# Optimization experiments

Hardware: AMD Instinct MI355X
Metric: run time of the kernel (lower is better)

## Reference

```python
import jax, jax.numpy as jnp
import numpy as np

B, TQ, TK, D, H = 4, 2048, 2048, 512, 8
NEG = -1e9
LN_EPS = 1e-3  # Keras LayerNormalization default


def setup_inputs() -> dict:
    key = jax.random.key(0)
    ks = jax.random.split(key, 5)
    s = 0.02
    return {
        "queries": jax.random.normal(ks[0], (B, TQ, D), jnp.float32),
        "keys_in": jax.random.normal(ks[1], (B, TK, D), jnp.float32),
        "Wq": jax.random.normal(ks[2], (D, D), jnp.float32) * s,
        "bq": jnp.zeros((D,), jnp.float32),
        "Wk": jax.random.normal(ks[3], (D, D), jnp.float32) * s,
        "bk": jnp.zeros((D,), jnp.float32),
        "Wv": jax.random.normal(ks[4], (D, D), jnp.float32) * s,
        "bv": jnp.zeros((D,), jnp.float32),
        "gamma": jnp.ones((D,), jnp.float32),
        "beta": jnp.zeros((D,), jnp.float32),
    }


def reference(queries, keys_in, Wq, bq, Wk, bk, Wv, bv, gamma, beta):
    # Dense projections with relu activation (as in the original layer)
    Q = jax.nn.relu(queries @ Wq + bq)   # [B, Tq, D]
    K = jax.nn.relu(keys_in @ Wk + bk)   # [B, Tk, D]
    V = jax.nn.relu(keys_in @ Wv + bv)   # [B, Tk, D]

    b, tq, d = Q.shape
    tk = K.shape[1]
    dh = d // H
    # split_heads: tf.split(axis=-1)+concat(axis=0) == contiguous feature chunks per head
    Qh = Q.reshape(b, tq, H, dh)
    Kh = K.reshape(b, tk, H, dh)
    Vh = V.reshape(b, tk, H, dh)

    scores = jnp.einsum('bqhd,bkhd->bhqk', Qh, Kh) / jnp.sqrt(jnp.float32(dh))

    # key padding mask derived from per-head K content: sum(|K|) > 0 along dh
    kmask = jnp.sum(jnp.abs(Kh), axis=-1) > 0            # [B, Tk, H]
    kmask = jnp.transpose(kmask, (0, 2, 1))              # [B, H, Tk]
    scores = jnp.where(kmask[:, :, None, :], scores, NEG)

    attn = jax.nn.softmax(scores, axis=-1)               # [B, H, Tq, Tk]

    # query mask: zero out attention rows for all-zero query positions
    qmask = (jnp.sum(jnp.abs(Qh), axis=-1) > 0).astype(attn.dtype)  # [B, Tq, H]
    qmask = jnp.transpose(qmask, (0, 2, 1))              # [B, H, Tq]
    attn = attn * qmask[:, :, :, None]

    out = jnp.einsum('bhqk,bkhd->bqhd', attn, Vh).reshape(b, tq, d)

    # residual + LayerNorm (Keras default: last axis, eps=1e-3)
    res = out + queries
    mu = jnp.mean(res, axis=-1, keepdims=True)
    var = jnp.var(res, axis=-1, keepdims=True)
    return (res - mu) * jax.lax.rsqrt(var + LN_EPS) * gamma + beta
```

## Files before the change

kernel.cpp:

```cpp
#include <hip/hip_runtime.h>
#include <cstdint>

#define BB 4
#define TT 2048
#define DD 512
#define HH 8
#define DH 64
#define NT (TT / 64)

using bf16x8 = __attribute__((ext_vector_type(8))) __bf16;
using f32x4  = __attribute__((ext_vector_type(4))) float;
using f32x16 = __attribute__((ext_vector_type(16))) float;
using us8    = __attribute__((ext_vector_type(8))) unsigned short;
using us4    = __attribute__((ext_vector_type(4))) unsigned short;
using u32x2  = __attribute__((ext_vector_type(2))) unsigned int;

typedef const __attribute__((address_space(1))) unsigned int* as1cp;
typedef __attribute__((address_space(3))) unsigned int* as3p;

__device__ __forceinline__ void gload16(const void* g, void* l) {
  __builtin_amdgcn_global_load_lds((as1cp)(uintptr_t)g,
                                   (as3p)(unsigned int)(uintptr_t)l, 16, 0, 0);
}

__device__ __forceinline__ unsigned short f2bf(float x) {
  unsigned int u = __float_as_uint(x);
  u += 0x7fffu + ((u >> 16) & 1u);
  return (unsigned short)(u >> 16);
}
__device__ __forceinline__ float bf2f(unsigned short u) {
  return __uint_as_float(((unsigned int)u) << 16);
}
__device__ __forceinline__ f32x4 MFMA(bf16x8 a, bf16x8 b, f32x4 c) {
  return __builtin_amdgcn_mfma_f32_16x16x32_bf16(a, b, c, 0, 0, 0);
}
__device__ __forceinline__ f32x16 MFMA32(bf16x8 a, bf16x8 b, f32x16 c) {
  return __builtin_amdgcn_mfma_f32_32x32x16_bf16(a, b, c, 0, 0, 0);
}
__device__ __forceinline__ unsigned int cvtpk(float lo, float hi) {
  unsigned int r;
  asm("v_cvt_pk_bf16_f32 %0, %1, %2" : "=v"(r) : "v"(lo), "v"(hi));
  return r;
}

#define WAITVM(N) asm volatile("s_waitcnt vmcnt(" #N ")" ::: "memory")
#define RAWBAR() asm volatile("s_barrier" ::: "memory")

__global__ __launch_bounds__(256) void cvt_inputs(const float4* __restrict__ q,
                                                  const float4* __restrict__ k,
                                                  us4* __restrict__ qb,
                                                  us4* __restrict__ kb) {
  size_t i = (size_t)blockIdx.x * 256 + threadIdx.x;
  float4 a = q[i];
  us4 o; o[0] = f2bf(a.x); o[1] = f2bf(a.y); o[2] = f2bf(a.z); o[3] = f2bf(a.w);
  qb[i] = o;
  float4 b = k[i];
  us4 p; p[0] = f2bf(b.x); p[1] = f2bf(b.y); p[2] = f2bf(b.z); p[3] = f2bf(b.w);
  kb[i] = p;
}

__global__ __launch_bounds__(256) void cvt_w(const float* __restrict__ Wq,
                                             const float* __restrict__ Wk,
                                             const float* __restrict__ Wv,
                                             unsigned short* __restrict__ Wt) {
  __shared__ float tile[32][33];
  int z = blockIdx.z;
  const float* W = (z == 0) ? Wq : (z == 1) ? Wk : Wv;
  int k0 = blockIdx.x * 32, n0 = blockIdx.y * 32;
  int r = threadIdx.x >> 5, c = threadIdx.x & 31;
#pragma unroll
  for (int p = 0; p < 4; ++p)
    tile[r + p * 8][c] = W[(size_t)(k0 + r + p * 8) * DD + n0 + c];
  __syncthreads();
  unsigned short* o = Wt + (size_t)z * DD * DD;
#pragma unroll
  for (int p = 0; p < 4; ++p)
    o[(size_t)(n0 + r + p * 8) * DD + k0 + c] = f2bf(tile[c][r + p * 8]);
}

__global__ __launch_bounds__(256) void gemm_proj(const unsigned short* __restrict__ qb,
                                                 const unsigned short* __restrict__ kb,
                                                 const unsigned short* __restrict__ Wt,
                                                 const float* __restrict__ bq,
                                                 const float* __restrict__ bk,
                                                 const float* __restrict__ bv,
                                                 unsigned short* __restrict__ Qp,
                                                 unsigned short* __restrict__ Kp,
                                                 unsigned short* __restrict__ Vp) {
  int z = blockIdx.z;
  const unsigned short* A  = (z == 0) ? qb : kb;
  const unsigned short* Bt = Wt + (size_t)z * DD * DD;
  const float* bias = (z == 0) ? bq : (z == 1) ? bk : bv;
  unsigned short* out = (z == 0) ? Qp : (z == 1) ? Kp : Vp;
  const float osc = (z == 0) ? 0.125f : 1.0f;

  __shared__ __align__(16) unsigned short As[128 * 32];
  __shared__ __align__(16) unsigned short Bs[128 * 32];

  int mb = blockIdx.x * 128, nb = blockIdx.y * 128;
  int w = threadIdx.x >> 6, lane = threadIdx.x & 63;
  int l15 = lane & 15, lg = lane >> 4;
  int wr = (w >> 1) * 64, wc = (w & 1) * 64;

  f32x4 acc[4][4] = {};

  for (int kt = 0; kt < DD / 32; ++kt) {
    int kk = kt * 32;
    int t = threadIdx.x;
#pragma unroll
    for (int it = 0; it < 2; ++it) {
      int c = t + it * 256;
      gload16(A  + (size_t)(mb + (c >> 2)) * DD + kk + (c & 3) * 8, As + c * 8);
      gload16(Bt + (size_t)(nb + (c >> 2)) * DD + kk + (c & 3) * 8, Bs + c * 8);
    }
    __syncthreads();
    bf16x8 af[4], bf[4];
#pragma unroll
    for (int m = 0; m < 4; ++m)
      af[m] = *(const bf16x8*)&As[(wr + m * 16 + l15) * 32 + lg * 8];
#pragma unroll
    for (int n = 0; n < 4; ++n)
      bf[n] = *(const bf16x8*)&Bs[(wc + n * 16 + l15) * 32 + lg * 8];
#pragma unroll
    for (int m = 0; m < 4; ++m)
#pragma unroll
      for (int n = 0; n < 4; ++n)
        acc[m][n] = MFMA(af[m], bf[n], acc[m][n]);
    __syncthreads();
  }

#pragma unroll
  for (int m = 0; m < 4; ++m)
#pragma unroll
    for (int n = 0; n < 4; ++n)
#pragma unroll
      for (int i = 0; i < 4; ++i) {
        int row = mb + wr + m * 16 + lg * 4 + i;
        int col = nb + wc + n * 16 + l15;
        float v = acc[m][n][i] + bias[col];
        out[(size_t)row * DD + col] = f2bf(fmaxf(v, 0.f) * osc);
      }
}

__global__ __launch_bounds__(256) void transpose_v(const unsigned short* __restrict__ Vp,
                                                   unsigned short* __restrict__ Vt) {
  __shared__ unsigned short tile[64][72];
  int b = blockIdx.z, k0 = blockIdx.x * 64, d0 = blockIdx.y * 64;
  int t = threadIdx.x;
  int r = t >> 3, c8 = (t & 7) * 8;
#pragma unroll
  for (int p = 0; p < 2; ++p) {
    int row = r + p * 32;
    us8 v = *(const us8*)&Vp[(size_t)(b * TT + k0 + row) * DD + d0 + c8];
#pragma unroll
    for (int j = 0; j < 8; ++j) tile[row][c8 + j] = v[j];
  }
  __syncthreads();
#pragma unroll
  for (int p = 0; p < 2; ++p) {
    int dr = r + p * 32;
    us8 o;
#pragma unroll
    for (int j = 0; j < 8; ++j) o[j] = tile[c8 + j][dr];
    *(us8*)&Vt[((size_t)b * DD + d0 + dr) * TT + k0 + c8] = o;
  }
}

__global__ __launch_bounds__(256) void mask_kernel(const unsigned short* __restrict__ Qp,
                                                   const unsigned short* __restrict__ Kp,
                                                   float* __restrict__ qmask,
                                                   uint2* __restrict__ kbits) {
  int id = blockIdx.x * 4 + (threadIdx.x >> 6);
  int lane = threadIdx.x & 63;
  int side = id >> 10;
  int rem = id & 1023;
  int bh = rem >> 5, tile = rem & 31;
  int b = bh >> 3, h = bh & 7;
  const unsigned short* src =
      (side ? Kp : Qp) + ((size_t)(b * TT + tile * 64 + lane)) * DD + h * DH;
  float s = 0.f;
#pragma unroll
  for (int j = 0; j < 64; j += 8) {
    us8 v = *(const us8*)(src + j);
#pragma unroll
    for (int e = 0; e < 8; ++e) s += bf2f(v[e]);
  }
  if (side == 0) {
    qmask[(size_t)bh * TT + tile * 64 + lane] = (s > 0.f) ? 1.f : 0.f;
  } else {
    unsigned long long mb = __ballot(s > 0.f);
    if (lane == 0)
      kbits[bh * NT + tile] = make_uint2((unsigned int)mb, (unsigned int)(mb >> 32));
  }
}

#define PV_SLOT(SS, base, ks)                                               \
  {                                                                         \
    unsigned int w0_ = cvtpk(SS[(base) + 0], SS[(base) + 1]);               \
    unsigned int w1_ = cvtpk(SS[(base) + 2], SS[(base) + 3]);               \
    unsigned int w2_ = cvtpk(SS[(base) + 4], SS[(base) + 5]);               \
    unsigned int w3_ = cvtpk(SS[(base) + 6], SS[(base) + 7]);               \
    u32x2 r20_ = __builtin_amdgcn_permlane32_swap(w2_, w0_, false, false);  \
    u32x2 r31_ = __builtin_amdgcn_permlane32_swap(w3_, w1_, false, false);  \
    union { unsigned int u[4]; bf16x8 v; } pa_;                             \
    pa_.u[0] = r20_[1]; pa_.u[1] = r31_[1];                                 \
    pa_.u[2] = r20_[0]; pa_.u[3] = r31_[0];                                 \
    oat0 = MFMA32(vf0[(ks)], pa_.v, oat0);                                  \
    oat1 = MFMA32(vf1[(ks)], pa_.v, oat1);                                  \
  }

#define STAGE(tt, pb)                                                        \
  {                                                                          \
    int c0_ = threadIdx.x;                                                   \
    _Pragma("unroll")                                                        \
    for (int it_ = 0; it_ < 2; ++it_) {                                      \
      int c_ = c0_ + it_ * 256;                                              \
      int r_ = c_ >> 3, j_ = c_ & 7;                                         \
      int js_ = j_ ^ (r_ & 7);                                               \
      gload16(kg + (size_t)((tt) * 64 + r_) * DD + js_ * 8,                  \
              &KsBuf[pb][(size_t)c_ * 8]);                                   \
      gload16(vg + (size_t)r_ * TT + (tt) * 64 + js_ * 8,                    \
              &VsBuf[pb][(size_t)c_ * 8]);                                   \
    }                                                                        \
  }

__global__ __launch_bounds__(256) void attn_kernel(
    const unsigned short* __restrict__ Qp,
    const unsigned short* __restrict__ Kp,
    const unsigned short* __restrict__ Vt,
    const uint2* __restrict__ kbits,
    const float* __restrict__ qmask,
    float* __restrict__ O) {
  __shared__ __align__(16) unsigned short KsBuf[2][64 * 64];
  __shared__ __align__(16) unsigned short VsBuf[2][64 * 64];

  const int w = threadIdx.x >> 6;
  const int lane = threadIdx.x & 63;
  const int l31 = lane & 31, h2 = lane >> 5;

  int flat = blockIdx.x;
  int wg = (flat & 7) * 64 + (flat >> 3);
  int qt = wg & 15, bh = wg >> 4;
  int h = bh & 7, b = bh >> 3;
  int q0 = qt * 128 + w * 32;

  const unsigned short* qbase =
      Qp + ((size_t)(b * TT + q0 + l31)) * DD + h * DH + h2 * 8;
  bf16x8 qf[4];
#pragma unroll
  for (int kd = 0; kd < 4; ++kd) qf[kd] = *(const bf16x8*)(qbase + kd * 16);

  const unsigned short* kg = Kp + ((size_t)b * TT) * DD + h * DH;
  const unsigned short* vg = Vt + ((size_t)(b * DD + h * DH)) * TT;
  const uint2* kb_ptr = kbits + (size_t)bh * NT;

  f32x16 oat0 = {}, oat1 = {};
  float m_i = -1e30f, l_i = 0.f;

  STAGE(0, 0);

  for (int t = 0; t < NT; ++t) {
    int pb = t & 1;
    if (t + 1 < NT) {
      STAGE(t + 1, pb ^ 1);
      WAITVM(4);
    } else {
      WAITVM(0);
    }
    RAWBAR();

    const unsigned short* ksb = &KsBuf[pb][0];
    const unsigned short* vsb = &VsBuf[pb][0];

    bf16x8 kf0[4], kf1[4];
#pragma unroll
    for (int kd = 0; kd < 4; ++kd) {
      int j = kd * 2 + h2;
      int r0 = l31, r1 = 32 + l31;
      kf0[kd] = *(const bf16x8*)&ksb[((size_t)r0 * 8 + (j ^ (r0 & 7))) * 8];
      kf1[kd] = *(const bf16x8*)&ksb[((size_t)r1 * 8 + (j ^ (r1 & 7))) * 8];
    }

    f32x16 s0 = {}, s1 = {};
    __builtin_amdgcn_s_setprio(1);
#pragma unroll
    for (int kd = 0; kd < 4; ++kd) s0 = MFMA32(kf0[kd], qf[kd], s0);
#pragma unroll
    for (int kd = 0; kd < 4; ++kd) s1 = MFMA32(kf1[kd], qf[kd], s1);
    __builtin_amdgcn_s_setprio(0);

    bf16x8 vf0[4], vf1[4];
#pragma unroll
    for (int ks = 0; ks < 4; ++ks) {
      int j = ks * 2 + h2;
      int r0 = l31, r1 = 32 + l31;
      vf0[ks] = *(const bf16x8*)&vsb[((size_t)r0 * 8 + (j ^ (r0 & 7))) * 8];
      vf1[ks] = *(const bf16x8*)&vsb[((size_t)r1 * 8 + (j ^ (r1 & 7))) * 8];
    }

    uint2 kw = kb_ptr[t];
    if ((kw.x & kw.y) != 0xffffffffu) {
      unsigned int w0s = kw.x >> (h2 * 4), w1s = kw.y >> (h2 * 4);
#pragma unroll
      for (int r = 0; r < 16; ++r) {
        int bi = (r & 3) + 8 * (r >> 2);
        if (!((w0s >> bi) & 1)) s0[r] = -1e30f;
        if (!((w1s >> bi) & 1)) s1[r] = -1e30f;
      }
    }

    float x0 = fmaxf(fmaxf(fmaxf(s0[0], s0[1]), fmaxf(s0[2], s0[3])),
                     fmaxf(fmaxf(s0[4], s0[5]), fmaxf(s0[6], s0[7])));
    float x1 = fmaxf(fmaxf(fmaxf(s0[8], s0[9]), fmaxf(s0[10], s0[11])),
                     fmaxf(fmaxf(s0[12], s0[13]), fmaxf(s0[14], s0[15])));
    float x2 = fmaxf(fmaxf(fmaxf(s1[0], s1[1]), fmaxf(s1[2], s1[3])),
                     fmaxf(fmaxf(s1[4], s1[5]), fmaxf(s1[6], s1[7])));
    float x3 = fmaxf(fmaxf(fmaxf(s1[8], s1[9]), fmaxf(s1[10], s1[11])),
                     fmaxf(fmaxf(s1[12], s1[13]), fmaxf(s1[14], s1[15])));
    float pm = fmaxf(fmaxf(x0, x1), fmaxf(x2, x3));
    u32x2 sw = __builtin_amdgcn_permlane32_swap(__float_as_uint(pm),
                                                __float_as_uint(pm), false, false);
    pm = fmaxf(__uint_as_float(sw[0]), __uint_as_float(sw[1]));

    if (__any(pm > m_i + 8.f)) {
      float mn = fmaxf(m_i, pm);
      float al = __expf(m_i - mn);
      m_i = mn;
      l_i *= al;
#pragma unroll
      for (int r = 0; r < 16; ++r) { oat0[r] *= al; oat1[r] *= al; }
    }

    float a0 = 0.f, a1 = 0.f, a2 = 0.f, a3 = 0.f;
#pragma unroll
    for (int r = 0; r < 8; ++r)  { float p = __expf(s0[r] - m_i); s0[r] = p; a0 += p; }
#pragma unroll
    for (int r = 8; r < 16; ++r) { float p = __expf(s0[r] - m_i); s0[r] = p; a1 += p; }
#pragma unroll
    for (int r = 0; r < 8; ++r)  { float p = __expf(s1[r] - m_i); s1[r] = p; a2 += p; }
#pragma unroll
    for (int r = 8; r < 16; ++r) { float p = __expf(s1[r] - m_i); s1[r] = p; a3 += p; }
    float rs = (a0 + a1) + (a2 + a3);
    u32x2 sr = __builtin_amdgcn_permlane32_swap(__float_as_uint(rs),
                                                __float_as_uint(rs), false, false);
    rs = __uint_as_float(sr[0]) + __uint_as_float(sr[1]);
    l_i += rs;

    __builtin_amdgcn_s_setprio(1);
    PV_SLOT(s0, 0, 0)
    PV_SLOT(s0, 8, 1)
    PV_SLOT(s1, 0, 2)
    PV_SLOT(s1, 8, 3)
    __builtin_amdgcn_s_setprio(0);

    if (t + 1 < NT) RAWBAR();
  }

  float qm = qmask[(size_t)bh * TT + q0 + l31];
  float sc = qm / l_i;
  float* ob = O + ((size_t)(b * TT + q0 + l31)) * DD + h * DH + h2 * 4;
#pragma unroll
  for (int qq = 0; qq < 4; ++qq) {
    float4 v0 = make_float4(oat0[4 * qq + 0] * sc, oat0[4 * qq + 1] * sc,
                            oat0[4 * qq + 2] * sc, oat0[4 * qq + 3] * sc);
    *(float4*)(ob + 8 * qq) = v0;
    float4 v1 = make_float4(oat1[4 * qq + 0] * sc, oat1[4 * qq + 1] * sc,
                            oat1[4 * qq + 2] * sc, oat1[4 * qq + 3] * sc);
    *(float4*)(ob + 32 + 8 * qq) = v1;
  }
}

__global__ __launch_bounds__(256) void ln_kernel(const float* __restrict__ O,
                                                 const float* __restrict__ qin,
                                                 const float* __restrict__ gamma,
                                                 const float* __restrict__ beta,
                                                 float* __restrict__ out) {
  int row = blockIdx.x * 4 + (threadIdx.x >> 6);
  int lane = threadIdx.x & 63;
  size_t base = (size_t)row * DD + lane * 8;
  const float4* o4 = (const float4*)(O + base);
  const float4* q4 = (const float4*)(qin + base);
  float4 a = o4[0], b2 = o4[1], c = q4[0], d2 = q4[1];
  float v[8];
  v[0] = a.x + c.x; v[1] = a.y + c.y; v[2] = a.z + c.z; v[3] = a.w + c.w;
  v[4] = b2.x + d2.x; v[5] = b2.y + d2.y; v[6] = b2.z + d2.z; v[7] = b2.w + d2.w;
  float s = 0.f, s2 = 0.f;
#pragma unroll
  for (int j = 0; j < 8; ++j) { s += v[j]; s2 += v[j] * v[j]; }
#pragma unroll
  for (int xm = 1; xm < 64; xm <<= 1) {
    s += __shfl_xor(s, xm);
    s2 += __shfl_xor(s2, xm);
  }
  float mu = s * (1.0f / DD);
  float var = s2 * (1.0f / DD) - mu * mu;
  float rs = rsqrtf(var + 1e-3f);
  const float* g = gamma + lane * 8;
  const float* bb = beta + lane * 8;
  float* ob = out + base;
#pragma unroll
  for (int j = 0; j < 8; ++j) ob[j] = (v[j] - mu) * rs * g[j] + bb[j];
}

extern "C" void kernel_launch(void* const* d_in, const int* in_sizes, int n_in,
                              void* d_out, int out_size, void* d_ws, size_t ws_size,
                              hipStream_t stream) {
  (void)in_sizes; (void)n_in; (void)out_size; (void)ws_size;
  const float* queries = (const float*)d_in[0];
  const float* keys_in = (const float*)d_in[1];
  const float* Wq = (const float*)d_in[2];
  const float* bq = (const float*)d_in[3];
  const float* Wk = (const float*)d_in[4];
  const float* bk = (const float*)d_in[5];
  const float* Wv = (const float*)d_in[6];
  const float* bv = (const float*)d_in[7];
  const float* gamma = (const float*)d_in[8];
  const float* beta  = (const float*)d_in[9];
  float* out = (float*)d_out;

  char* ws = (char*)d_ws;
  unsigned short* qb = (unsigned short*)(ws);
  unsigned short* kb = (unsigned short*)(ws + (8ull << 20));
  float*          O  = (float*)(ws);
  unsigned short* Qp = (unsigned short*)(ws + (16ull << 20));
  unsigned short* Kp = (unsigned short*)(ws + (24ull << 20));
  unsigned short* Vp = (unsigned short*)(ws + (32ull << 20));
  unsigned short* Vt = (unsigned short*)(ws + (40ull << 20));
  unsigned short* Wt = (unsigned short*)(ws + (48ull << 20));
  float* qmaskp = (float*)(ws + (50ull << 20));
  uint2* kbitsp = (uint2*)(ws + (50ull << 20) + (512ull << 10));

  cvt_inputs<<<4096, 256, 0, stream>>>((const float4*)queries, (const float4*)keys_in,
                                       (us4*)qb, (us4*)kb);
  cvt_w<<<dim3(16, 16, 3), 256, 0, stream>>>(Wq, Wk, Wv, Wt);
  gemm_proj<<<dim3(64, 4, 3), 256, 0, stream>>>(qb, kb, Wt, bq, bk, bv, Qp, Kp, Vp);
  transpose_v<<<dim3(32, 8, 4), 256, 0, stream>>>(Vp, Vt);
  mask_kernel<<<512, 256, 0, stream>>>(Qp, Kp, qmaskp, kbitsp);
  attn_kernel<<<512, 256, 0, stream>>>(Qp, Kp, Vt, kbitsp, qmaskp, O);
  ln_kernel<<<2048, 256, 0, stream>>>(O, queries, gamma, beta, out);
}
```

Before: 193.8 us.

## Switch attention to 16x16 MFMA tiles, exp2 softmax, and merge small prep kernels

Replaces the 32x32x16 MFMA attention inner loop with 16x16x32 tiles. Each wave now handles 16 queries instead of 32, so the launch grows to 1024 blocks of 64 queries each. Softmax moves to exp2 by folding log2(e) into the Q scale, with a clamp and a larger rescale threshold. Separately, the input/weight conversion kernels are merged into one launch, and the V transpose and mask kernels into another, to cut launch overhead. The smaller tiles give more parallelism but lower per-wave reuse of K/V tiles and more LDS traffic.

```diff
diff --git a/kernel.cpp b/kernel.cpp
--- a/kernel.cpp
+++ b/kernel.cpp
@@ -7,10 +7,10 @@
 #define HH 8
 #define DH 64
 #define NT (TT / 64)
+#define LOG2E 1.4426950408889634f
 
 using bf16x8 = __attribute__((ext_vector_type(8))) __bf16;
 using f32x4  = __attribute__((ext_vector_type(4))) float;
-using f32x16 = __attribute__((ext_vector_type(16))) float;
 using us8    = __attribute__((ext_vector_type(8))) unsigned short;
 using us4    = __attribute__((ext_vector_type(4))) unsigned short;
 using u32x2  = __attribute__((ext_vector_type(2))) unsigned int;
@@ -34,48 +34,43 @@
 __device__ __forceinline__ f32x4 MFMA(bf16x8 a, bf16x8 b, f32x4 c) {
   return __builtin_amdgcn_mfma_f32_16x16x32_bf16(a, b, c, 0, 0, 0);
 }
-__device__ __forceinline__ f32x16 MFMA32(bf16x8 a, bf16x8 b, f32x16 c) {
-  return __builtin_amdgcn_mfma_f32_32x32x16_bf16(a, b, c, 0, 0, 0);
-}
-__device__ __forceinline__ unsigned int cvtpk(float lo, float hi) {
-  unsigned int r;
-  asm("v_cvt_pk_bf16_f32 %0, %1, %2" : "=v"(r) : "v"(lo), "v"(hi));
-  return r;
-}
 
 #define WAITVM(N) asm volatile("s_waitcnt vmcnt(" #N ")" ::: "memory")
 #define RAWBAR() asm volatile("s_barrier" ::: "memory")
 
-__global__ __launch_bounds__(256) void cvt_inputs(const float4* __restrict__ q,
-                                                  const float4* __restrict__ k,
-                                                  us4* __restrict__ qb,
-                                                  us4* __restrict__ kb) {
-  size_t i = (size_t)blockIdx.x * 256 + threadIdx.x;
-  float4 a = q[i];
-  us4 o; o[0] = f2bf(a.x); o[1] = f2bf(a.y); o[2] = f2bf(a.z); o[3] = f2bf(a.w);
-  qb[i] = o;
-  float4 b = k[i];
-  us4 p; p[0] = f2bf(b.x); p[1] = f2bf(b.y); p[2] = f2bf(b.z); p[3] = f2bf(b.w);
-  kb[i] = p;
-}
-
-__global__ __launch_bounds__(256) void cvt_w(const float* __restrict__ Wq,
-                                             const float* __restrict__ Wk,
-                                             const float* __restrict__ Wv,
-                                             unsigned short* __restrict__ Wt) {
+__global__ __launch_bounds__(256) void prep_kernel(const float4* __restrict__ q,
+                                                   const float4* __restrict__ k,
+                                                   us4* __restrict__ qb,
+                                                   us4* __restrict__ kb,
+                                                   const float* __restrict__ Wq,
+                                                   const float* __restrict__ Wk,
+                                                   const float* __restrict__ Wv,
+                                                   unsigned short* __restrict__ Wt) {
   __shared__ float tile[32][33];
-  int z = blockIdx.z;
-  const float* W = (z == 0) ? Wq : (z == 1) ? Wk : Wv;
-  int k0 = blockIdx.x * 32, n0 = blockIdx.y * 32;
-  int r = threadIdx.x >> 5, c = threadIdx.x & 31;
-#pragma unroll
-  for (int p = 0; p < 4; ++p)
-    tile[r + p * 8][c] = W[(size_t)(k0 + r + p * 8) * DD + n0 + c];
-  __syncthreads();
-  unsigned short* o = Wt + (size_t)z * DD * DD;
-#pragma unroll
-  for (int p = 0; p < 4; ++p)
-    o[(size_t)(n0 + r + p * 8) * DD + k0 + c] = f2bf(tile[c][r + p * 8]);
+  int id = blockIdx.x;
+  if (id < 4096) {
+    size_t i = (size_t)id * 256 + threadIdx.x;
+    float4 a = q[i];
+    us4 o; o[0] = f2bf(a.x); o[1] = f2bf(a.y); o[2] = f2bf(a.z); o[3] = f2bf(a.w);
+    qb[i] = o;
+    float4 b = k[i];
+    us4 p; p[0] = f2bf(b.x); p[1] = f2bf(b.y); p[2] = f2bf(b.z); p[3] = f2bf(b.w);
+    kb[i] = p;
+  } else {
+    int id2 = id - 4096;
+    int z = id2 >> 8, rem = id2 & 255;
+    const float* W = (z == 0) ? Wq : (z == 1) ? Wk : Wv;
+    int k0 = (rem & 15) * 32, n0 = (rem >> 4) * 32;
+    int r = threadIdx.x >> 5, c = threadIdx.x & 31;
+#pragma unroll
+    for (int p = 0; p < 4; ++p)
+      tile[r + p * 8][c] = W[(size_t)(k0 + r + p * 8) * DD + n0 + c];
+    __syncthreads();
+    unsigned short* o = Wt + (size_t)z * DD * DD;
+#pragma unroll
+    for (int p = 0; p < 4; ++p)
+      o[(size_t)(n0 + r + p * 8) * DD + k0 + c] = f2bf(tile[c][r + p * 8]);
+  }
 }
 
 __global__ __launch_bounds__(256) void gemm_proj(const unsigned short* __restrict__ qb,
@@ -92,7 +87,7 @@
   const unsigned short* Bt = Wt + (size_t)z * DD * DD;
   const float* bias = (z == 0) ? bq : (z == 1) ? bk : bv;
   unsigned short* out = (z == 0) ? Qp : (z == 1) ? Kp : Vp;
-  const float osc = (z == 0) ? 0.125f : 1.0f;
+  const float osc = (z == 0) ? 0.125f * LOG2E : 1.0f;
 
   __shared__ __align__(16) unsigned short As[128 * 32];
   __shared__ __align__(16) unsigned short Bs[128 * 32];
@@ -142,74 +137,61 @@
       }
 }
 
-__global__ __launch_bounds__(256) void transpose_v(const unsigned short* __restrict__ Vp,
-                                                   unsigned short* __restrict__ Vt) {
+__global__ __launch_bounds__(256) void post_proj(const unsigned short* __restrict__ Qp,
+                                                 const unsigned short* __restrict__ Kp,
+                                                 const unsigned short* __restrict__ Vp,
+                                                 unsigned short* __restrict__ Vt,
+                                                 float* __restrict__ qmask,
+                                                 uint2* __restrict__ kbits) {
   __shared__ unsigned short tile[64][72];
-  int b = blockIdx.z, k0 = blockIdx.x * 64, d0 = blockIdx.y * 64;
-  int t = threadIdx.x;
-  int r = t >> 3, c8 = (t & 7) * 8;
-#pragma unroll
-  for (int p = 0; p < 2; ++p) {
-    int row = r + p * 32;
-    us8 v = *(const us8*)&Vp[(size_t)(b * TT + k0 + row) * DD + d0 + c8];
-#pragma unroll
-    for (int j = 0; j < 8; ++j) tile[row][c8 + j] = v[j];
-  }
-  __syncthreads();
-#pragma unroll
-  for (int p = 0; p < 2; ++p) {
-    int dr = r + p * 32;
-    us8 o;
-#pragma unroll
-    for (int j = 0; j < 8; ++j) o[j] = tile[c8 + j][dr];
-    *(us8*)&Vt[((size_t)b * DD + d0 + dr) * TT + k0 + c8] = o;
-  }
-}
-
-__global__ __launch_bounds__(256) void mask_kernel(const unsigned short* __restrict__ Qp,
-                                                   const unsigned short* __restrict__ Kp,
-                                                   float* __restrict__ qmask,
-                                                   uint2* __restrict__ kbits) {
-  int id = blockIdx.x * 4 + (threadIdx.x >> 6);
-  int lane = threadIdx.x & 63;
-  int side = id >> 10;
-  int rem = id & 1023;
-  int bh = rem >> 5, tile = rem & 31;
-  int b = bh >> 3, h = bh & 7;
-  const unsigned short* src =
-      (side ? Kp : Qp) + ((size_t)(b * TT + tile * 64 + lane)) * DD + h * DH;
-  float s = 0.f;
-#pragma unroll
-  for (int j = 0; j < 64; j += 8) {
-    us8 v = *(const us8*)(src + j);
-#pragma unroll
-    for (int e = 0; e < 8; ++e) s += bf2f(v[e]);
-  }
-  if (side == 0) {
-    qmask[(size_t)bh * TT + tile * 64 + lane] = (s > 0.f) ? 1.f : 0.f;
+  int id = blockIdx.x;
+  if (id < 1024) {
+    int b = id >> 8, k0 = (id & 31) * 64, d0 = ((id >> 5) & 7) * 64;
+    int t = threadIdx.x;
+    int r = t >> 3, c8 = (t & 7) * 8;
+#pragma unroll
+    for (int p = 0; p < 2; ++p) {
+      int row = r + p * 32;
+      us8 v = *(const us8*)&Vp[(size_t)(b * TT + k0 + row) * DD + d0 + c8];
+#pragma unroll
+      for (int j = 0; j < 8; ++j) tile[row][c8 + j] = v[j];
+    }
+    __syncthreads();
+#pragma unroll
+    for (int p = 0; p < 2; ++p) {
+      int dr = r + p * 32;
+      us8 o;
+#pragma unroll
+      for (int j = 0; j < 8; ++j) o[j] = tile[c8 + j][dr];
+      *(us8*)&Vt[((size_t)b * DD + d0 + dr) * TT + k0 + c8] = o;
+    }
   } else {
-    unsigned long long mb = __ballot(s > 0.f);
-    if (lane == 0)
-      kbits[bh * NT + tile] = make_uint2((unsigned int)mb, (unsigned int)(mb >> 32));
-  }
-}
-
-#define PV_SLOT(SS, base, ks)                                               \
-  {                                                                         \
-    unsigned int w0_ = cvtpk(SS[(base) + 0], SS[(base) + 1]);               \
-    unsigned int w1_ = cvtpk(SS[(base) + 2], SS[(base) + 3]);               \
-    unsigned int w2_ = cvtpk(SS[(base) + 4], SS[(base) + 5]);               \
-    unsigned int w3_ = cvtpk(SS[(base) + 6], SS[(base) + 7]);               \
-    u32x2 r20_ = __builtin_amdgcn_permlane32_swap(w2_, w0_, false, false);  \
-    u32x2 r31_ = __builtin_amdgcn_permlane32_swap(w3_, w1_, false, false);  \
-    union { unsigned int u[4]; bf16x8 v; } pa_;                             \
-    pa_.u[0] = r20_[1]; pa_.u[1] = r31_[1];                                 \
-    pa_.u[2] = r20_[0]; pa_.u[3] = r31_[0];                                 \
-    oat0 = MFMA32(vf0[(ks)], pa_.v, oat0);                                  \
-    oat1 = MFMA32(vf1[(ks)], pa_.v, oat1);                                  \
-  }
-
-#define STAGE(tt, pb)                                                        \
+    int wid = (id - 1024) * 4 + (threadIdx.x >> 6);
+    int lane = threadIdx.x & 63;
+    int side = wid >> 10;
+    int rem = wid & 1023;
+    int bh = rem >> 5, tl = rem & 31;
+    int b = bh >> 3, h = bh & 7;
+    const unsigned short* src =
+        (side ? Kp : Qp) + ((size_t)(b * TT + tl * 64 + lane)) * DD + h * DH;
+    float s = 0.f;
+#pragma unroll
+    for (int j = 0; j < 64; j += 8) {
+      us8 v = *(const us8*)(src + j);
+#pragma unroll
+      for (int e = 0; e < 8; ++e) s += bf2f(v[e]);
+    }
+    if (side == 0) {
+      qmask[(size_t)bh * TT + tl * 64 + lane] = (s > 0.f) ? 1.f : 0.f;
+    } else {
+      unsigned long long mb = __ballot(s > 0.f);
+      if (lane == 0)
+        kbits[bh * NT + tl] = make_uint2((unsigned int)mb, (unsigned int)(mb >> 32));
+    }
+  }
+}
+
+#define STAGE(tt, pbuf)                                                      \
   {                                                                          \
     int c0_ = threadIdx.x;                                                   \
     _Pragma("unroll")                                                        \
@@ -218,9 +200,9 @@
       int r_ = c_ >> 3, j_ = c_ & 7;                                         \
       int js_ = j_ ^ (r_ & 7);                                               \
       gload16(kg + (size_t)((tt) * 64 + r_) * DD + js_ * 8,                  \
-              &KsBuf[pb][(size_t)c_ * 8]);                                   \
+              &KsBuf[pbuf][(size_t)c_ * 8]);                                 \
       gload16(vg + (size_t)r_ * TT + (tt) * 64 + js_ * 8,                    \
-              &VsBuf[pb][(size_t)c_ * 8]);                                   \
+              &VsBuf[pbuf][(size_t)c_ * 8]);                                 \
     }                                                                        \
   }
 
@@ -236,25 +218,26 @@
 
   const int w = threadIdx.x >> 6;
   const int lane = threadIdx.x & 63;
-  const int l31 = lane & 31, h2 = lane >> 5;
+  const int l15 = lane & 15, lg = lane >> 4;
 
   int flat = blockIdx.x;
-  int wg = (flat & 7) * 64 + (flat >> 3);
-  int qt = wg & 15, bh = wg >> 4;
+  int wg = (flat & 7) * 128 + (flat >> 3);
+  int qt = wg & 31, bh = wg >> 5;
   int h = bh & 7, b = bh >> 3;
-  int q0 = qt * 128 + w * 32;
+  int q0 = qt * 64 + w * 16;
 
   const unsigned short* qbase =
-      Qp + ((size_t)(b * TT + q0 + l31)) * DD + h * DH + h2 * 8;
-  bf16x8 qf[4];
-#pragma unroll
-  for (int kd = 0; kd < 4; ++kd) qf[kd] = *(const bf16x8*)(qbase + kd * 16);
+      Qp + ((size_t)(b * TT + q0 + l15)) * DD + h * DH + lg * 8;
+  bf16x8 qf0 = *(const bf16x8*)(qbase);
+  bf16x8 qf1 = *(const bf16x8*)(qbase + 32);
 
   const unsigned short* kg = Kp + ((size_t)b * TT) * DD + h * DH;
   const unsigned short* vg = Vt + ((size_t)(b * DD + h * DH)) * TT;
   const uint2* kb_ptr = kbits + (size_t)bh * NT;
 
-  f32x16 oat0 = {}, oat1 = {};
+  const int krow_base = ((l15 & 12) << 1) | (l15 & 3);
+
+  f32x4 oat[4] = {};
   float m_i = -1e30f, l_i = 0.f;
 
   STAGE(0, 0);
@@ -272,101 +255,105 @@
     const unsigned short* ksb = &KsBuf[pb][0];
     const unsigned short* vsb = &VsBuf[pb][0];
 
-    bf16x8 kf0[4], kf1[4];
-#pragma unroll
-    for (int kd = 0; kd < 4; ++kd) {
-      int j = kd * 2 + h2;
-      int r0 = l31, r1 = 32 + l31;
-      kf0[kd] = *(const bf16x8*)&ksb[((size_t)r0 * 8 + (j ^ (r0 & 7))) * 8];
-      kf1[kd] = *(const bf16x8*)&ksb[((size_t)r1 * 8 + (j ^ (r1 & 7))) * 8];
-    }
-
-    f32x16 s0 = {}, s1 = {};
+    f32x4 s[4];
     __builtin_amdgcn_s_setprio(1);
 #pragma unroll
-    for (int kd = 0; kd < 4; ++kd) s0 = MFMA32(kf0[kd], qf[kd], s0);
-#pragma unroll
-    for (int kd = 0; kd < 4; ++kd) s1 = MFMA32(kf1[kd], qf[kd], s1);
+    for (int f = 0; f < 4; ++f) {
+      int row = krow_base + ((f & 1) << 2) + ((f >> 1) << 5);
+      int r7 = row & 7;
+      bf16x8 k0 = *(const bf16x8*)&ksb[row * 64 + ((lg ^ r7) << 3)];
+      bf16x8 k1 = *(const bf16x8*)&ksb[row * 64 + (((4 | lg) ^ r7) << 3)];
+      f32x4 z = {};
+      z = MFMA(k0, qf0, z);
+      s[f] = MFMA(k1, qf1, z);
+    }
     __builtin_amdgcn_s_setprio(0);
 
-    bf16x8 vf0[4], vf1[4];
-#pragma unroll
-    for (int ks = 0; ks < 4; ++ks) {
-      int j = ks * 2 + h2;
-      int r0 = l31, r1 = 32 + l31;
-      vf0[ks] = *(const bf16x8*)&vsb[((size_t)r0 * 8 + (j ^ (r0 & 7))) * 8];
-      vf1[ks] = *(const bf16x8*)&vsb[((size_t)r1 * 8 + (j ^ (r1 & 7))) * 8];
+    bf16x8 vf[4][2];
+#pragma unroll
+    for (int fd = 0; fd < 4; ++fd) {
+      int row = 16 * fd + l15;
+      int r7 = l15 & 7;
+      vf[fd][0] = *(const bf16x8*)&vsb[row * 64 + ((lg ^ r7) << 3)];
+      vf[fd][1] = *(const bf16x8*)&vsb[row * 64 + (((4 | lg) ^ r7) << 3)];
     }
 
     uint2 kw = kb_ptr[t];
     if ((kw.x & kw.y) != 0xffffffffu) {
-      unsigned int w0s = kw.x >> (h2 * 4), w1s = kw.y >> (h2 * 4);
-#pragma unroll
-      for (int r = 0; r < 16; ++r) {
-        int bi = (r & 3) + 8 * (r >> 2);
-        if (!((w0s >> bi) & 1)) s0[r] = -1e30f;
-        if (!((w1s >> bi) & 1)) s1[r] = -1e30f;
+#pragma unroll
+      for (int f = 0; f < 4; ++f) {
+        unsigned int word = (f >> 1) ? kw.y : kw.x;
+        unsigned int nib = (word >> (8 * lg + 4 * (f & 1))) & 0xFu;
+#pragma unroll
+        for (int i = 0; i < 4; ++i)
+          if (!((nib >> i) & 1)) s[f][i] = -1e30f;
       }
     }
 
-    float x0 = fmaxf(fmaxf(fmaxf(s0[0], s0[1]), fmaxf(s0[2], s0[3])),
-                     fmaxf(fmaxf(s0[4], s0[5]), fmaxf(s0[6], s0[7])));
-    float x1 = fmaxf(fmaxf(fmaxf(s0[8], s0[9]), fmaxf(s0[10], s0[11])),
-                     fmaxf(fmaxf(s0[12], s0[13]), fmaxf(s0[14], s0[15])));
-    float x2 = fmaxf(fmaxf(fmaxf(s1[0], s1[1]), fmaxf(s1[2], s1[3])),
-                     fmaxf(fmaxf(s1[4], s1[5]), fmaxf(s1[6], s1[7])));
-    float x3 = fmaxf(fmaxf(fmaxf(s1[8], s1[9]), fmaxf(s1[10], s1[11])),
-                     fmaxf(fmaxf(s1[12], s1[13]), fmaxf(s1[14], s1[15])));
-    float pm = fmaxf(fmaxf(x0, x1), fmaxf(x2, x3));
+    float m0 = fmaxf(fmaxf(s[0][0], s[0][1]), fmaxf(s[0][2], s[0][3]));
+    float m1 = fmaxf(fmaxf(s[1][0], s[1][1]), fmaxf(s[1][2], s[1][3]));
+    float m2 = fmaxf(fmaxf(s[2][0], s[2][1]), fmaxf(s[2][2], s[2][3]));
+    float m3 = fmaxf(fmaxf(s[3][0], s[3][1]), fmaxf(s[3][2], s[3][3]));
+    float pm = fmaxf(fmaxf(m0, m1), fmaxf(m2, m3));
+    pm = fmaxf(pm, __shfl_xor(pm, 16));
     u32x2 sw = __builtin_amdgcn_permlane32_swap(__float_as_uint(pm),
                                                 __float_as_uint(pm), false, false);
     pm = fmaxf(__uint_as_float(sw[0]), __uint_as_float(sw[1]));
 
-    if (__any(pm > m_i + 8.f)) {
+    if (__any(pm > m_i + 12.f)) {
       float mn = fmaxf(m_i, pm);
-      float al = __expf(m_i - mn);
+      float al = exp2f(m_i - mn);
       m_i = mn;
       l_i *= al;
 #pragma unroll
-      for (int r = 0; r < 16; ++r) { oat0[r] *= al; oat1[r] *= al; }
-    }
-
-    float a0 = 0.f, a1 = 0.f, a2 = 0.f, a3 = 0.f;
-#pragma unroll
-    for (int r = 0; r < 8; ++r)  { float p = __expf(s0[r] - m_i); s0[r] = p; a0 += p; }
-#pragma unroll
-    for (int r = 8; r < 16; ++r) { float p = __expf(s0[r] - m_i); s0[r] = p; a1 += p; }
-#pragma unroll
-    for (int r = 0; r < 8; ++r)  { float p = __expf(s1[r] - m_i); s1[r] = p; a2 += p; }
-#pragma unroll
-    for (int r = 8; r < 16; ++r) { float p = __expf(s1[r] - m_i); s1[r] = p; a3 += p; }
-    float rs = (a0 + a1) + (a2 + a3);
-    u32x2 sr = __builtin_amdgcn_permlane32_swap(__float_as_uint(rs),
-                                                __float_as_uint(rs), false, false);
-    rs = __uint_as_float(sr[0]) + __uint_as_float(sr[1]);
-    l_i += rs;
+      for (int f = 0; f < 4; ++f)
+#pragma unroll
+        for (int i = 0; i < 4; ++i) oat[f][i] *= al;
+    }
+
+    float a = 0.f;
+#pragma unroll
+    for (int f = 0; f < 4; ++f)
+#pragma unroll
+      for (int i = 0; i < 4; ++i) {
+        float p = exp2f(fminf(s[f][i] - m_i, 30.f));
+        s[f][i] = p;
+        a += p;
+      }
+    a += __shfl_xor(a, 16);
+    u32x2 sr = __builtin_amdgcn_permlane32_swap(__float_as_uint(a),
+                                                __float_as_uint(a), false, false);
+    a = __uint_as_float(sr[0]) + __uint_as_float(sr[1]);
+    l_i += a;
+
+    bf16x8 pb0v, pb1v;
+#pragma unroll
+    for (int f2 = 0; f2 < 2; ++f2)
+#pragma unroll
+      for (int i = 0; i < 4; ++i) {
+        pb0v[f2 * 4 + i] = (__bf16)s[f2][i];
+        pb1v[f2 * 4 + i] = (__bf16)s[2 + f2][i];
+      }
 
     __builtin_amdgcn_s_setprio(1);
-    PV_SLOT(s0, 0, 0)
-    PV_SLOT(s0, 8, 1)
-    PV_SLOT(s1, 0, 2)
-    PV_SLOT(s1, 8, 3)
+#pragma unroll
+    for (int fd = 0; fd < 4; ++fd) {
+      oat[fd] = MFMA(vf[fd][0], pb0v, oat[fd]);
+      oat[fd] = MFMA(vf[fd][1], pb1v, oat[fd]);
+    }
     __builtin_amdgcn_s_setprio(0);
 
     if (t + 1 < NT) RAWBAR();
   }
 
-  float qm = qmask[(size_t)bh * TT + q0 + l31];
-  float sc = qm / l_i;
-  float* ob = O + ((size_t)(b * TT + q0 + l31)) * DD + h * DH + h2 * 4;
-#pragma unroll
-  for (int qq = 0; qq < 4; ++qq) {
-    float4 v0 = make_float4(oat0[4 * qq + 0] * sc, oat0[4 * qq + 1] * sc,
-                            oat0[4 * qq + 2] * sc, oat0[4 * qq + 3] * sc);
-    *(float4*)(ob + 8 * qq) = v0;
-    float4 v1 = make_float4(oat1[4 * qq + 0] * sc, oat1[4 * qq + 1] * sc,
-                            oat1[4 * qq + 2] * sc, oat1[4 * qq + 3] * sc);
-    *(float4*)(ob + 32 + 8 * qq) = v1;
+  float qm = qmask[(size_t)bh * TT + q0 + l15];
+  float sc = qm / fmaxf(l_i, 1e-37f);
+  float* ob = O + ((size_t)(b * TT + q0 + l15)) * DD + h * DH + 4 * lg;
+#pragma unroll
+  for (int fd = 0; fd < 4; ++fd) {
+    float4 v = make_float4(oat[fd][0] * sc, oat[fd][1] * sc,
+                           oat[fd][2] * sc, oat[fd][3] * sc);
+    *(float4*)(ob + 16 * fd) = v;
   }
 }
 
@@ -430,12 +417,10 @@
   float* qmaskp = (float*)(ws + (50ull << 20));
   uint2* kbitsp = (uint2*)(ws + (50ull << 20) + (512ull << 10));
 
-  cvt_inputs<<<4096, 256, 0, stream>>>((const float4*)queries, (const float4*)keys_in,
-                                       (us4*)qb, (us4*)kb);
-  cvt_w<<<dim3(16, 16, 3), 256, 0, stream>>>(Wq, Wk, Wv, Wt);
+  prep_kernel<<<4864, 256, 0, stream>>>((const float4*)queries, (const float4*)keys_in,
+                                        (us4*)qb, (us4*)kb, Wq, Wk, Wv, Wt);
   gemm_proj<<<dim3(64, 4, 3), 256, 0, stream>>>(qb, kb, Wt, bq, bk, bv, Qp, Kp, Vp);
-  transpose_v<<<dim3(32, 8, 4), 256, 0, stream>>>(Vp, Vt);
-  mask_kernel<<<512, 256, 0, stream>>>(Qp, Kp, qmaskp, kbitsp);
-  attn_kernel<<<512, 256, 0, stream>>>(Qp, Kp, Vt, kbitsp, qmaskp, O);
+  post_proj<<<1536, 256, 0, stream>>>(Qp, Kp, Vp, Vt, qmaskp, kbitsp);
+  attn_kernel<<<1024, 256, 0, stream>>>(Qp, Kp, Vt, kbitsp, qmaskp, O);
   ln_kernel<<<2048, 256, 0, stream>>>(O, queries, gamma, beta, out);
 }
```

After: 216.0 us. +11.4%, slower.
